# Performance work log

Hardware: AMD Instinct MI355X
Metric: run time of the kernel (lower is better)

The kernel has to match this reference:

```python
import jax, jax.numpy as jnp
import numpy as np

N = 50000      # nodes
E = 800000     # directed edges (avg degree 16)
F_IN = 128     # dataset.num_features
H = 256        # hidden_channels
C = 40         # dataset.num_classes


def _glorot(k, shape):
    lim = float(np.sqrt(6.0 / (shape[0] + shape[1])))
    return jax.random.uniform(k, shape, jnp.float32, -lim, lim)


def setup_inputs() -> dict:
    key = jax.random.key(0)
    ks = jax.random.split(key, 8)
    x = jax.random.normal(ks[0], (N, F_IN), jnp.float32)
    edge_index = jax.random.randint(ks[1], (2, E), 0, N, dtype=jnp.int32)
    W1 = _glorot(ks[2], (F_IN, H));      b1 = jnp.zeros((H,), jnp.float32)
    W2 = _glorot(ks[3], (H, H // 2));    b2 = jnp.zeros((H // 2,), jnp.float32)
    W3 = _glorot(ks[4], (H // 2, H // 4)); b3 = jnp.zeros((H // 4,), jnp.float32)
    W4 = _glorot(ks[5], (H // 4, C));    b4 = jnp.zeros((C,), jnp.float32)
    return {"x": x, "edge_index": edge_index,
            "W1": W1, "b1": b1, "W2": W2, "b2": b2,
            "W3": W3, "b3": b3, "W4": W4, "b4": b4}


def reference(x, edge_index, W1, b1, W2, b2, W3, b3, W4, b4):
    # GCNConv with default add_self_loops=True and symmetric normalization.
    loops = jnp.arange(N, dtype=edge_index.dtype)
    src = jnp.concatenate([edge_index[0], loops])   # message sources
    dst = jnp.concatenate([edge_index[1], loops])   # aggregation targets
    # degree computed on target index (PyG default), incl. self-loops
    deg = jax.ops.segment_sum(jnp.ones_like(dst, jnp.float32), dst, num_segments=N)
    dinv = jnp.where(deg > 0, jax.lax.rsqrt(deg), 0.0)
    norm = dinv[src] * dinv[dst]                    # [E+N]

    def conv(h, W, b):
        h = h @ W                                   # transform first (PyG order)
        msg = h[src] * norm[:, None]                # gather + scale
        return jax.ops.segment_sum(msg, dst, num_segments=N) + b

    h = jax.nn.relu(conv(x, W1, b1))   # dropout = identity in eval mode
    h = jax.nn.relu(conv(h, W2, b2))
    h = jax.nn.relu(conv(h, W3, b3))
    return conv(h, W4, b4)
```

## Files before the change

### kernel.cpp

```cpp
#include <hip/hip_runtime.h>
#include <stdint.h>

#define NNODES 50000
#define NEDGES 800000
#define NB ((NNODES + 255) / 256)
#define EPB 4096
#define SCAT_NBLK ((NEDGES + EPB - 1) / EPB)

typedef __attribute__((ext_vector_type(8))) short bf16x8;
typedef __attribute__((ext_vector_type(4))) float f32x4;

__device__ inline unsigned short f2bf(float f) {
    unsigned u = __float_as_uint(f);
    return (unsigned short)((u + 0x7fffu + ((u >> 16) & 1u)) >> 16);
}
__device__ inline float bf2f(unsigned short h) {
    return __uint_as_float(((unsigned)h) << 16);
}


__global__ void zero_kernel(int* __restrict__ p, int n) {
    int i = blockIdx.x * blockDim.x + threadIdx.x;
    if (i < n) p[i] = 0;
}

__global__ __launch_bounds__(256) void bucket_count_kernel(const int* __restrict__ dst,
                                                           int* __restrict__ bhist) {
    __shared__ int h[NB];
    for (int b = threadIdx.x; b < NB; b += 256) h[b] = 0;
    __syncthreads();
    const int base = blockIdx.x * EPB;
#pragma unroll
    for (int i = 0; i < EPB / 256; ++i) {
        const int e = base + threadIdx.x + i * 256;
        if (e < NEDGES) atomicAdd(&h[dst[e] >> 8], 1);
    }
    __syncthreads();
    for (int b = threadIdx.x; b < NB; b += 256)
        if (h[b]) atomicAdd(&bhist[b], h[b]);
}

__global__ __launch_bounds__(256) void bucket_scan_kernel(const int* __restrict__ bhist,
                                                          int* __restrict__ bofs,
                                                          int* __restrict__ gcur,
                                                          int* __restrict__ rp_last) {
    __shared__ int s[256];
    const int t = threadIdx.x;
    s[t] = (t < NB) ? bhist[t] : 0;
    __syncthreads();
    for (int off = 1; off < 256; off <<= 1) {
        int v = (t >= off) ? s[t - off] : 0;
        __syncthreads();
        s[t] += v;
        __syncthreads();
    }
    if (t < NB) {
        const int excl = (t > 0) ? s[t - 1] : 0;
        bofs[t] = excl;
        gcur[t] = excl;
    }
    if (t == 255) { bofs[NB] = s[255]; rp_last[0] = s[255]; }
}

__global__ __launch_bounds__(256) void bucket_scatter_kernel(const int* __restrict__ src,
                                                             const int* __restrict__ dst,
                                                             int* __restrict__ gcur,
                                                             unsigned* __restrict__ gpk) {
    __shared__ int h[256];
    __shared__ int s[256];
    __shared__ int gof[256];
    __shared__ unsigned pr[EPB];
    __shared__ int ga[EPB];

    const int t = threadIdx.x;
    const int base = blockIdx.x * EPB;
    const int nval = min(EPB, NEDGES - base);

    h[t] = 0;
    __syncthreads();
#pragma unroll
    for (int i = 0; i < EPB / 256; ++i) {
        const int e = base + t + i * 256;
        if (e < NEDGES) atomicAdd(&h[dst[e] >> 8], 1);
    }
    __syncthreads();
    s[t] = h[t];
    __syncthreads();
    for (int off = 1; off < 256; off <<= 1) {
        int v = (t >= off) ? s[t - off] : 0;
        __syncthreads();
        s[t] += v;
        __syncthreads();
    }
    {
        const int c = h[t];
        if (t < NB && c > 0) gof[t] = atomicAdd(&gcur[t], c);
        const int lofs = s[t] - c;
        h[t] = lofs;
        s[t] = lofs;
    }
    __syncthreads();
#pragma unroll
    for (int i = 0; i < EPB / 256; ++i) {
        const int e = base + t + i * 256;
        if (e < NEDGES) {
            const int d = dst[e];
            const int b = d >> 8;
            const int slot = atomicAdd(&h[b], 1);
            pr[slot] = ((unsigned)(d & 255) << 16) | (unsigned)src[e];
            ga[slot] = gof[b] + (slot - s[b]);
        }
    }
    __syncthreads();
#pragma unroll
    for (int i = 0; i < EPB / 256; ++i) {
        const int slot = t + i * 256;
        if (slot < nval) gpk[ga[slot]] = pr[slot];
    }
}

__global__ __launch_bounds__(256) void csr_fill_kernel(const unsigned* __restrict__ gpk,
                                                       const int* __restrict__ bofs,
                                                       int* __restrict__ rp,
                                                       float* __restrict__ dinv,
                                                       unsigned short* __restrict__ col,
                                                       const float* __restrict__ x,
                                                       unsigned short* __restrict__ xbf) {
    __shared__ int c[256];
    __shared__ int s[256];
    __shared__ int cur[256];
    __shared__ float sdv[256];
    const int t = threadIdx.x;
    const int b = blockIdx.x;
    const int beg = bofs[b], end = bofs[b + 1];
    c[t] = 0;
    __syncthreads();
    for (int e = beg + t; e < end; e += 256) atomicAdd(&c[gpk[e] >> 16], 1);
    __syncthreads();
    s[t] = c[t];
    __syncthreads();
    for (int off = 1; off < 256; off <<= 1) {
        int v = (t >= off) ? s[t - off] : 0;
        __syncthreads();
        s[t] += v;
        __syncthreads();
    }
    const int excl = s[t] - c[t];
    cur[t] = excl;
    const int node = b * 256 + t;
    const float dv = rsqrtf((float)(c[t] + 1));
    sdv[t] = dv;
    if (node < NNODES) {
        rp[node] = beg + excl;
        dinv[node] = dv;
    }
    __syncthreads();
    for (int e = beg + t; e < end; e += 256) {
        const unsigned p = gpk[e];
        const int r = atomicAdd(&cur[p >> 16], 1);
        col[beg + r] = (unsigned short)(p & 0xffffu);
    }
    const int nrows = min(256, NNODES - b * 256);
    const float* xb = x + (size_t)b * 256 * 128;
    unsigned short* ob = xbf + (size_t)b * 256 * 128;
    const int n4 = nrows * 32;
    for (int i = t; i < n4; i += 256) {
        const float dv2 = sdv[i >> 5];
        float4 v = *(const float4*)(xb + (size_t)i * 4);
        ushort4 hh;
        hh.x = f2bf(dv2 * v.x); hh.y = f2bf(dv2 * v.y);
        hh.z = f2bf(dv2 * v.z); hh.w = f2bf(dv2 * v.w);
        *(ushort4*)(ob + (size_t)i * 4) = hh;
    }
}


template <bool RELU, bool HAS_BIAS, bool WRITE_SPLIT>
__global__ __launch_bounds__(256) void agg128_kernel(const float* __restrict__ in32,
                                                     const unsigned short* __restrict__ inbf,
                                                     float* __restrict__ out,
                                                     unsigned short* __restrict__ outhi,
                                                     unsigned short* __restrict__ outlo,
                                                     const int* __restrict__ rp,
                                                     const unsigned short* __restrict__ col,
                                                     const float* __restrict__ dinv,
                                                     const float* __restrict__ bias) {
    const int wave = threadIdx.x >> 6;
    const int lane = threadIdx.x & 63;
    const int d = blockIdx.x * 4 + wave;
    if (d >= NNODES) return;
    const int quarter = lane >> 4;
    const int fl = lane & 15;
    const float dv = dinv[d];

    float acc[8] = {0.f, 0.f, 0.f, 0.f, 0.f, 0.f, 0.f, 0.f};
    if (quarter == 0) {
        float4 s0 = *(const float4*)(in32 + (size_t)d * 128 + fl * 8);
        float4 s1 = *(const float4*)(in32 + (size_t)d * 128 + fl * 8 + 4);
        acc[0] = dv * s0.x; acc[1] = dv * s0.y; acc[2] = dv * s0.z; acc[3] = dv * s0.w;
        acc[4] = dv * s1.x; acc[5] = dv * s1.y; acc[6] = dv * s1.z; acc[7] = dv * s1.w;
    }

    int j = rp[d] + quarter;
    const int end = rp[d + 1];
    for (; j + 12 < end; j += 16) {
        const int c0 = col[j], c1 = col[j + 4], c2 = col[j + 8], c3 = col[j + 12];
        bf16x8 a0 = *(const bf16x8*)(inbf + (size_t)c0 * 128 + fl * 8);
        bf16x8 a1 = *(const bf16x8*)(inbf + (size_t)c1 * 128 + fl * 8);
        bf16x8 a2 = *(const bf16x8*)(inbf + (size_t)c2 * 128 + fl * 8);
        bf16x8 a3 = *(const bf16x8*)(inbf + (size_t)c3 * 128 + fl * 8);
#pragma unroll
        for (int k = 0; k < 8; ++k)
            acc[k] += (bf2f((unsigned short)a0[k]) + bf2f((unsigned short)a1[k])) +
                      (bf2f((unsigned short)a2[k]) + bf2f((unsigned short)a3[k]));
    }
    for (; j + 4 < end; j += 8) {
        const int c0 = col[j], c1 = col[j + 4];
        bf16x8 a0 = *(const bf16x8*)(inbf + (size_t)c0 * 128 + fl * 8);
        bf16x8 a1 = *(const bf16x8*)(inbf + (size_t)c1 * 128 + fl * 8);
#pragma unroll
        for (int k = 0; k < 8; ++k)
            acc[k] += bf2f((unsigned short)a0[k]) + bf2f((unsigned short)a1[k]);
    }
    if (j < end) {
        const int c0 = col[j];
        bf16x8 a0 = *(const bf16x8*)(inbf + (size_t)c0 * 128 + fl * 8);
#pragma unroll
        for (int k = 0; k < 8; ++k) acc[k] += bf2f((unsigned short)a0[k]);
    }

#pragma unroll
    for (int v = 0; v < 8; ++v) {
        acc[v] += __shfl_down(acc[v], 32);
        acc[v] += __shfl_down(acc[v], 16);
    }

    if (quarter == 0) {
        float r[8];
#pragma unroll
        for (int v = 0; v < 8; ++v) {
            float t = dv * acc[v];
            if constexpr (HAS_BIAS) t += bias[fl * 8 + v];
            if constexpr (RELU) t = fmaxf(t, 0.0f);
            r[v] = t;
        }
        if constexpr (WRITE_SPLIT) {
            ushort4 h0, h1v, l0, l1v;
            h0.x = f2bf(r[0]); l0.x = f2bf(r[0] - bf2f(h0.x));
            h0.y = f2bf(r[1]); l0.y = f2bf(r[1] - bf2f(h0.y));
            h0.z = f2bf(r[2]); l0.z = f2bf(r[2] - bf2f(h0.z));
            h0.w = f2bf(r[3]); l0.w = f2bf(r[3] - bf2f(h0.w));
            h1v.x = f2bf(r[4]); l1v.x = f2bf(r[4] - bf2f(h1v.x));
            h1v.y = f2bf(r[5]); l1v.y = f2bf(r[5] - bf2f(h1v.y));
            h1v.z = f2bf(r[6]); l1v.z = f2bf(r[6] - bf2f(h1v.z));
            h1v.w = f2bf(r[7]); l1v.w = f2bf(r[7] - bf2f(h1v.w));
            *(ushort4*)(outhi + (size_t)d * 128 + fl * 8)     = h0;
            *(ushort4*)(outhi + (size_t)d * 128 + fl * 8 + 4) = h1v;
            *(ushort4*)(outlo + (size_t)d * 128 + fl * 8)     = l0;
            *(ushort4*)(outlo + (size_t)d * 128 + fl * 8 + 4) = l1v;
        } else {
            *(float4*)(out + (size_t)d * 128 + fl * 8)     = make_float4(r[0], r[1], r[2], r[3]);
            *(float4*)(out + (size_t)d * 128 + fl * 8 + 4) = make_float4(r[4], r[5], r[6], r[7]);
        }
    }
}

template <bool RELU, bool HAS_BIAS, bool WRITE_BF>
__global__ __launch_bounds__(256) void agg64_kernel(const float* __restrict__ in32,
                                                    const unsigned short* __restrict__ inbf,
                                                    float* __restrict__ out,
                                                    unsigned short* __restrict__ outbf,
                                                    const int* __restrict__ rp,
                                                    const unsigned short* __restrict__ col,
                                                    const float* __restrict__ dinv,
                                                    const float* __restrict__ bias) {
    const int wave = threadIdx.x >> 6;
    const int lane = threadIdx.x & 63;
    const int d = blockIdx.x * 4 + wave;
    if (d >= NNODES) return;
    const int eighth = lane >> 3;
    const int fl = lane & 7;
    const float dv = dinv[d];

    float acc[8] = {0.f, 0.f, 0.f, 0.f, 0.f, 0.f, 0.f, 0.f};
    if (eighth == 0) {
        float4 s0 = *(const float4*)(in32 + (size_t)d * 64 + fl * 8);
        float4 s1 = *(const float4*)(in32 + (size_t)d * 64 + fl * 8 + 4);
        acc[0] = dv * s0.x; acc[1] = dv * s0.y; acc[2] = dv * s0.z; acc[3] = dv * s0.w;
        acc[4] = dv * s1.x; acc[5] = dv * s1.y; acc[6] = dv * s1.z; acc[7] = dv * s1.w;
    }

    int j = rp[d] + eighth;
    const int end = rp[d + 1];
    for (; j + 8 < end; j += 16) {
        const int c0 = col[j], c1 = col[j + 8];
        bf16x8 a0 = *(const bf16x8*)(inbf + (size_t)c0 * 64 + fl * 8);
        bf16x8 a1 = *(const bf16x8*)(inbf + (size_t)c1 * 64 + fl * 8);
#pragma unroll
        for (int k = 0; k < 8; ++k)
            acc[k] += bf2f((unsigned short)a0[k]) + bf2f((unsigned short)a1[k]);
    }
    if (j < end) {
        const int c0 = col[j];
        bf16x8 a0 = *(const bf16x8*)(inbf + (size_t)c0 * 64 + fl * 8);
#pragma unroll
        for (int k = 0; k < 8; ++k) acc[k] += bf2f((unsigned short)a0[k]);
    }

#pragma unroll
    for (int v = 0; v < 8; ++v) {
        acc[v] += __shfl_down(acc[v], 32);
        acc[v] += __shfl_down(acc[v], 16);
        acc[v] += __shfl_down(acc[v], 8);
    }

    if (eighth == 0) {
        float r[8];
#pragma unroll
        for (int v = 0; v < 8; ++v) {
            float t = dv * acc[v];
            if constexpr (HAS_BIAS) t += bias[fl * 8 + v];
            if constexpr (RELU) t = fmaxf(t, 0.0f);
            r[v] = t;
        }
        *(float4*)(out + (size_t)d * 64 + fl * 8)     = make_float4(r[0], r[1], r[2], r[3]);
        *(float4*)(out + (size_t)d * 64 + fl * 8 + 4) = make_float4(r[4], r[5], r[6], r[7]);
        if constexpr (WRITE_BF) {
            ushort4 h0, h1;
            h0.x = f2bf(dv * r[0]); h0.y = f2bf(dv * r[1]);
            h0.z = f2bf(dv * r[2]); h0.w = f2bf(dv * r[3]);
            h1.x = f2bf(dv * r[4]); h1.y = f2bf(dv * r[5]);
            h1.z = f2bf(dv * r[6]); h1.w = f2bf(dv * r[7]);
            *(ushort4*)(outbf + (size_t)d * 64 + fl * 8)     = h0;
            *(ushort4*)(outbf + (size_t)d * 64 + fl * 8 + 4) = h1;
        }
    }
}


template <int K, int M>
__global__ __launch_bounds__(256) void repack_kernel(const float* __restrict__ W,
                                                     unsigned short* __restrict__ hi,
                                                     unsigned short* __restrict__ lo) {
    int i = blockIdx.x * 256 + threadIdx.x;
    if (i >= K * M) return;
    const int k = i / M, n = i % M;
    constexpr int KS = K / 32;
    const int cb = n >> 7;
    const int ct = (n >> 4) & 7;
    const int ln = ((k >> 3) & 3) * 16 + (n & 15);
    const int j  = k & 7;
    const int ks = k >> 5;
    const size_t o = ((((size_t)cb * KS + ks) * 8 + ct) * 64 + ln) * 8 + j;
    const float f = W[i];
    const unsigned short h = f2bf(f);
    hi[o] = h;
    lo[o] = f2bf(f - bf2f(h));
}


template <int K, int M, int EPI>
__global__ __launch_bounds__(256) void mfma2_kernel(const unsigned short* __restrict__ Ahi_g,
                                                    const unsigned short* __restrict__ Alo_g,
                                                    const unsigned short* __restrict__ Whi,
                                                    const unsigned short* __restrict__ Wlo,
                                                    const float* __restrict__ bias,
                                                    float* __restrict__ C,
                                                    unsigned short* __restrict__ Chi,
                                                    unsigned short* __restrict__ Clo,
                                                    unsigned short* __restrict__ Cbf,
                                                    const float* __restrict__ dinv) {
    constexpr int KS = K / 32;
    constexpr int CI = M / 64;
    __shared__ char lds[8192];
    char* Ahi = lds;
    char* Alo = lds + 4096;

    const int t = threadIdx.x;
    const int lane = t & 63;
    const int w = t >> 6;
    const int r0 = blockIdx.x * 64;
    const int quad = lane >> 4;
    const int cl = lane & 15;

    const size_t abase = ((size_t)(r0 + w * 16 + cl) * K + (size_t)quad * 8) * 2;

    f32x4 acc[4][CI];
#pragma unroll
    for (int i = 0; i < 4; ++i)
#pragma unroll
        for (int j = 0; j < CI; ++j) acc[i][j] = (f32x4){0.f, 0.f, 0.f, 0.f};

    for (int ks = 0; ks < KS; ++ks) {
        const size_t koff = abase + (size_t)ks * 64;
        __builtin_amdgcn_global_load_lds(
            (const __attribute__((address_space(1))) void*)((const char*)Ahi_g + koff),
            (__attribute__((address_space(3))) void*)(Ahi + w * 1024), 16, 0, 0);
        __builtin_amdgcn_global_load_lds(
            (const __attribute__((address_space(1))) void*)((const char*)Alo_g + koff),
            (__attribute__((address_space(3))) void*)(Alo + w * 1024), 16, 0, 0);

        bf16x8 bh[CI], bl[CI];
#pragma unroll
        for (int j = 0; j < CI; ++j) {
            const int g = w * CI + j;
            const size_t off = (size_t)(((g >> 3) * KS + ks) * 8 + (g & 7)) * 512 + lane * 8;
            bh[j] = *(const bf16x8*)(Whi + off);
            bl[j] = *(const bf16x8*)(Wlo + off);
        }
        __syncthreads();

        bf16x8 ah[4], al[4];
#pragma unroll
        for (int i = 0; i < 4; ++i) {
            ah[i] = *(const bf16x8*)(Ahi + i * 1024 + lane * 16);
            al[i] = *(const bf16x8*)(Alo + i * 1024 + lane * 16);
        }
#pragma unroll
        for (int i = 0; i < 4; ++i)
#pragma unroll
            for (int j = 0; j < CI; ++j) {
                acc[i][j] = __builtin_amdgcn_mfma_f32_16x16x32_bf16(ah[i], bh[j], acc[i][j], 0, 0, 0);
                acc[i][j] = __builtin_amdgcn_mfma_f32_16x16x32_bf16(ah[i], bl[j], acc[i][j], 0, 0, 0);
                acc[i][j] = __builtin_amdgcn_mfma_f32_16x16x32_bf16(al[i], bh[j], acc[i][j], 0, 0, 0);
            }
        __syncthreads();
    }

#pragma unroll
    for (int i = 0; i < 4; ++i)
#pragma unroll
        for (int j = 0; j < CI; ++j) {
            const int colg = (w * CI + j) * 16 + cl;
            float bv = 0.f;
            if constexpr (EPI == 0) bv = bias[colg];
#pragma unroll
            for (int r = 0; r < 4; ++r) {
                const int rowg = r0 + i * 16 + quad * 4 + r;
                if (rowg < NNODES) {
                    if constexpr (EPI == 0) {
                        const float v = fmaxf(acc[i][j][r] + bv, 0.f);
                        const unsigned short h = f2bf(v);
                        Chi[(size_t)rowg * M + colg] = h;
                        Clo[(size_t)rowg * M + colg] = f2bf(v - bf2f(h));
                    } else {
                        const float v = acc[i][j][r];
                        C[(size_t)rowg * M + colg] = v;
                        Cbf[(size_t)rowg * M + colg] = f2bf(dinv[rowg] * v);
                    }
                }
            }
        }
}


template <int BM, int BN, int BK, int TM, int TN, bool HAS_BIAS, bool RELU, bool WRITE_BF>
__global__ __launch_bounds__(256) void gemm_kernel(const float* __restrict__ A,
                                                   const float* __restrict__ W,
                                                   const float* __restrict__ bias,
                                                   float* __restrict__ C,
                                                   unsigned short* __restrict__ Cbf,
                                                   const float* __restrict__ dinv,
                                                   int Nrows, int K, int M) {
    constexpr int TX = BN / TN;
    constexpr int TY = BM / TM;
    static_assert(TX * TY == 256, "thread grid must be 256");
    constexpr int A_LOADS = (BM * BK) / (256 * 4);
    constexpr int W_LOADS = (BN * BK) / (256 * 4);
    static_assert(A_LOADS >= 1 && W_LOADS >= 1, "tile too small");

    const int tid = threadIdx.x;
    const int tx = tid % TX;
    const int ty = tid / TX;
    const int r0 = blockIdx.x * BM;
    const int c0 = blockIdx.y * BN;

    __shared__ float As[BK][BM + 4];
    __shared__ float Ws[BK][BN];

    float acc[TM][TN] = {};

    for (int k0 = 0; k0 < K; k0 += BK) {
#pragma unroll
        for (int l = 0; l < A_LOADS; ++l) {
            const int idx = tid + l * 256;
            const int row = idx / (BK / 4);
            const int kq = idx % (BK / 4);
            float4 v = make_float4(0.f, 0.f, 0.f, 0.f);
            const int gr = r0 + row;
            if (gr < Nrows) v = *(const float4*)(A + (size_t)gr * K + k0 + kq * 4);
            As[kq * 4 + 0][row] = v.x;
            As[kq * 4 + 1][row] = v.y;
            As[kq * 4 + 2][row] = v.z;
            As[kq * 4 + 3][row] = v.w;
        }
#pragma unroll
        for (int l = 0; l < W_LOADS; ++l) {
            const int idx = tid + l * 256;
            const int kk = idx / (BN / 4);
            const int cq = idx % (BN / 4);
            const int gc = c0 + cq * 4;
            float4 v;
            const float* wrow = W + (size_t)(k0 + kk) * M;
            if (gc + 3 < M) {
                v = *(const float4*)(wrow + gc);
            } else {
                v.x = (gc + 0 < M) ? wrow[gc + 0] : 0.f;
                v.y = (gc + 1 < M) ? wrow[gc + 1] : 0.f;
                v.z = (gc + 2 < M) ? wrow[gc + 2] : 0.f;
                v.w = (gc + 3 < M) ? wrow[gc + 3] : 0.f;
            }
            *(float4*)&Ws[kk][cq * 4] = v;
        }
        __syncthreads();

#pragma unroll
        for (int kk = 0; kk < BK; ++kk) {
            float a[TM], b[TN];
#pragma unroll
            for (int i = 0; i < TM; ++i) a[i] = As[kk][ty * TM + i];
#pragma unroll
            for (int j = 0; j < TN; ++j) b[j] = Ws[kk][tx * TN + j];
#pragma unroll
            for (int i = 0; i < TM; ++i)
#pragma unroll
                for (int j = 0; j < TN; ++j) acc[i][j] += a[i] * b[j];
        }
        __syncthreads();
    }

#pragma unroll
    for (int i = 0; i < TM; ++i) {
        const int gr = r0 + ty * TM + i;
        if (gr >= Nrows) continue;
        const float dvr = WRITE_BF ? dinv[gr] : 0.f;
#pragma unroll
        for (int j = 0; j < TN; ++j) {
            const int gc = c0 + tx * TN + j;
            if (gc >= M) continue;
            float v = acc[i][j];
            if constexpr (HAS_BIAS) v += bias[gc];
            if constexpr (RELU) v = fmaxf(v, 0.0f);
            C[(size_t)gr * M + gc] = v;
            if constexpr (WRITE_BF) Cbf[(size_t)gr * M + gc] = f2bf(dvr * v);
        }
    }
}


extern "C" void kernel_launch(void* const* d_in, const int* in_sizes, int n_in,
                              void* d_out, int out_size, void* d_ws, size_t ws_size,
                              hipStream_t stream) {
    const float* x  = (const float*)d_in[0];
    const int* ei   = (const int*)d_in[1];
    const float* W1 = (const float*)d_in[2];
    const float* b1 = (const float*)d_in[3];
    const float* W2 = (const float*)d_in[4];
    const float* b2 = (const float*)d_in[5];
    const float* W3 = (const float*)d_in[6];
    const float* b3 = (const float*)d_in[7];
    const float* W4 = (const float*)d_in[8];
    const float* b4 = (const float*)d_in[9];
    float* out = (float*)d_out;
    const int* esrc = ei;
    const int* edst = ei + NEDGES;

    char* w = (char*)d_ws;
    auto alloc = [&](size_t bytes) -> void* {
        void* p = (void*)w;
        w += (bytes + 255) & ~(size_t)255;
        return p;
    };
    int* rp     = (int*)alloc((size_t)(NNODES + 1) * 4);
    unsigned short* col = (unsigned short*)alloc((size_t)NEDGES * 2);
    float* dinv = (float*)alloc((size_t)NNODES * 4);
    int* bhist  = (int*)alloc((size_t)NB * 4);
    int* bofs   = (int*)alloc((size_t)(NB + 1) * 4);
    int* gcur   = (int*)alloc((size_t)NB * 4);
    unsigned* gpk = (unsigned*)alloc((size_t)NEDGES * 4);
    unsigned short* W1hi = (unsigned short*)alloc((size_t)128 * 256 * 2);
    unsigned short* W1lo = (unsigned short*)alloc((size_t)128 * 256 * 2);
    unsigned short* W2hi = (unsigned short*)alloc((size_t)256 * 128 * 2);
    unsigned short* W2lo = (unsigned short*)alloc((size_t)256 * 128 * 2);
    unsigned short* AggHi = (unsigned short*)alloc((size_t)NNODES * 128 * 2);
    unsigned short* AggLo = (unsigned short*)alloc((size_t)NNODES * 128 * 2);
    unsigned short* H1hi  = (unsigned short*)alloc((size_t)NNODES * 256 * 2);
    unsigned short* H1lo  = (unsigned short*)alloc((size_t)NNODES * 256 * 2);
    float* B0   = (float*)alloc((size_t)NNODES * 64 * 4);
    float* B1   = (float*)alloc((size_t)NNODES * 128 * 4);
    float* B2   = (float*)alloc((size_t)NNODES * 128 * 4);
    unsigned short* xbf  = (unsigned short*)alloc((size_t)NNODES * 128 * 2);
    unsigned short* B1bf = (unsigned short*)alloc((size_t)NNODES * 128 * 2);
    unsigned short* B0bf = (unsigned short*)alloc((size_t)NNODES * 64 * 2);
    unsigned short* B3bf = (unsigned short*)alloc((size_t)NNODES * 64 * 2);

    repack_kernel<128, 256><<<(128 * 256 + 255) / 256, 256, 0, stream>>>(W1, W1hi, W1lo);
    repack_kernel<256, 128><<<(256 * 128 + 255) / 256, 256, 0, stream>>>(W2, W2hi, W2lo);

    zero_kernel<<<1, 256, 0, stream>>>(bhist, NB);
    bucket_count_kernel<<<SCAT_NBLK, 256, 0, stream>>>(edst, bhist);
    bucket_scan_kernel<<<1, 256, 0, stream>>>(bhist, bofs, gcur, rp + NNODES);
    bucket_scatter_kernel<<<SCAT_NBLK, 256, 0, stream>>>(esrc, edst, gcur, gpk);
    csr_fill_kernel<<<NB, 256, 0, stream>>>(gpk, bofs, rp, dinv, col, x, xbf);

    const int aggGrid = (NNODES + 3) / 4;
    const int rowBlks64 = (NNODES + 63) / 64;

    agg128_kernel<false, false, true><<<aggGrid, 256, 0, stream>>>(
        x, xbf, nullptr, AggHi, AggLo, rp, col, dinv, nullptr);
    mfma2_kernel<128, 256, 0><<<rowBlks64, 256, 0, stream>>>(
        AggHi, AggLo, W1hi, W1lo, b1, nullptr, H1hi, H1lo, nullptr, nullptr);
    mfma2_kernel<256, 128, 1><<<rowBlks64, 256, 0, stream>>>(
        H1hi, H1lo, W2hi, W2lo, nullptr, B1, nullptr, nullptr, B1bf, dinv);
    agg128_kernel<true, true, false><<<aggGrid, 256, 0, stream>>>(
        B1, B1bf, B2, nullptr, nullptr, rp, col, dinv, b2);

    gemm_kernel<64, 64, 16, 4, 4, false, false, true>
        <<<dim3(rowBlks64, 1), 256, 0, stream>>>(B2, W3, nullptr, B0, B0bf, dinv, NNODES, 128, 64);
    agg64_kernel<true, true, true><<<aggGrid, 256, 0, stream>>>(B0, B0bf, B1, B3bf, rp, col, dinv, b3);

    agg64_kernel<false, false, false><<<aggGrid, 256, 0, stream>>>(B1, B3bf, B2, nullptr, rp, col, dinv, nullptr);
    gemm_kernel<64, 64, 16, 4, 4, true, false, false>
        <<<dim3(rowBlks64, 1), 256, 0, stream>>>(B2, W4, b4, out, nullptr, nullptr, NNODES, 64, 40);
}
```

Baseline: 355.5 us.

## Stage weight tiles in LDS and split MFMA GEMM over column blocks

The split-bf16 MFMA GEMM now loads weight fragments into LDS with global_load_lds instead of per-wave register loads from global memory. It also tiles the output columns in blocks of 128 via a 2D grid, so layer 1 launches twice as many blocks with half the accumulators each. The A tile is now loaded with coalesced ushort4 reads and row-bounds checks, then swizzled into LDS. The aim is more parallelism and lower register pressure for the larger GEMM, at the cost of extra LDS use and reading A twice in layer 1.

```diff
diff --git a/kernel.cpp b/kernel.cpp
--- a/kernel.cpp
+++ b/kernel.cpp
@@ -360,30 +360,32 @@
 
 
 template <int K, int M, int EPI>
-__global__ __launch_bounds__(256) void mfma2_kernel(const unsigned short* __restrict__ Ahi_g,
-                                                    const unsigned short* __restrict__ Alo_g,
-                                                    const unsigned short* __restrict__ Whi,
-                                                    const unsigned short* __restrict__ Wlo,
-                                                    const float* __restrict__ bias,
-                                                    float* __restrict__ C,
-                                                    unsigned short* __restrict__ Chi,
-                                                    unsigned short* __restrict__ Clo,
-                                                    unsigned short* __restrict__ Cbf,
-                                                    const float* __restrict__ dinv) {
+__global__ __launch_bounds__(256) void mfma_sb_kernel(const unsigned short* __restrict__ Ahi_g,
+                                                      const unsigned short* __restrict__ Alo_g,
+                                                      const unsigned short* __restrict__ Whi,
+                                                      const unsigned short* __restrict__ Wlo,
+                                                      const float* __restrict__ bias,
+                                                      float* __restrict__ C,
+                                                      unsigned short* __restrict__ Chi,
+                                                      unsigned short* __restrict__ Clo,
+                                                      unsigned short* __restrict__ Cbf,
+                                                      const float* __restrict__ dinv) {
     constexpr int KS = K / 32;
-    constexpr int CI = M / 64;
-    __shared__ char lds[8192];
+    constexpr int CI = 2;
+    __shared__ char lds[8192 + 16384];
     char* Ahi = lds;
     char* Alo = lds + 4096;
+    char* Bhi = lds + 8192;
+    char* Blo = lds + 16384;
 
     const int t = threadIdx.x;
     const int lane = t & 63;
     const int w = t >> 6;
     const int r0 = blockIdx.x * 64;
-    const int quad = lane >> 4;
-    const int cl = lane & 15;
-
-    const size_t abase = ((size_t)(r0 + w * 16 + cl) * K + (size_t)quad * 8) * 2;
+    const int n0 = blockIdx.y * 128;
+
+    const unsigned short* bhg = Whi + (size_t)blockIdx.y * KS * 4096;
+    const unsigned short* blg = Wlo + (size_t)blockIdx.y * KS * 4096;
 
     f32x4 acc[4][CI];
 #pragma unroll
@@ -392,29 +394,60 @@
         for (int j = 0; j < CI; ++j) acc[i][j] = (f32x4){0.f, 0.f, 0.f, 0.f};
 
     for (int ks = 0; ks < KS; ++ks) {
-        const size_t koff = abase + (size_t)ks * 64;
-        __builtin_amdgcn_global_load_lds(
-            (const __attribute__((address_space(1))) void*)((const char*)Ahi_g + koff),
-            (__attribute__((address_space(3))) void*)(Ahi + w * 1024), 16, 0, 0);
-        __builtin_amdgcn_global_load_lds(
-            (const __attribute__((address_space(1))) void*)((const char*)Alo_g + koff),
-            (__attribute__((address_space(3))) void*)(Alo + w * 1024), 16, 0, 0);
-
-        bf16x8 bh[CI], bl[CI];
-#pragma unroll
-        for (int j = 0; j < CI; ++j) {
-            const int g = w * CI + j;
-            const size_t off = (size_t)(((g >> 3) * KS + ks) * 8 + (g & 7)) * 512 + lane * 8;
-            bh[j] = *(const bf16x8*)(Whi + off);
-            bl[j] = *(const bf16x8*)(Wlo + off);
-        }
-        __syncthreads();
-
-        bf16x8 ah[4], al[4];
+        const int k0 = ks * 32;
+
+        {
+            const char* gh = (const char*)(bhg + (size_t)ks * 4096);
+            const char* gl = (const char*)(blg + (size_t)ks * 4096);
+#pragma unroll
+            for (int c = 0; c < 2; ++c) {
+                const int ct = w * 2 + c;
+                __builtin_amdgcn_global_load_lds(
+                    (const __attribute__((address_space(1))) void*)(gh + ct * 1024 + lane * 16),
+                    (__attribute__((address_space(3))) void*)(Bhi + ct * 1024), 16, 0, 0);
+                __builtin_amdgcn_global_load_lds(
+                    (const __attribute__((address_space(1))) void*)(gl + ct * 1024 + lane * 16),
+                    (__attribute__((address_space(3))) void*)(Blo + ct * 1024), 16, 0, 0);
+            }
+        }
+
+        ushort4 hv[2], lv[2];
+#pragma unroll
+        for (int i = 0; i < 2; ++i) {
+            const int q = t + i * 256;
+            const int row = q >> 3;
+            const int kq = (q & 7) * 4;
+            const int gr = r0 + row;
+            ushort4 h = {0, 0, 0, 0}, l = {0, 0, 0, 0};
+            if (gr < NNODES) {
+                h = *(const ushort4*)(Ahi_g + (size_t)gr * K + k0 + kq);
+                l = *(const ushort4*)(Alo_g + (size_t)gr * K + k0 + kq);
+            }
+            hv[i] = h;
+            lv[i] = l;
+        }
+#pragma unroll
+        for (int i = 0; i < 2; ++i) {
+            const int q = t + i * 256;
+            const int row = q >> 3;
+            const int kq = (q & 7) * 4;
+            const int rt = row >> 4, m = row & 15, quad = kq >> 3, j0 = kq & 7;
+            const int off = rt * 1024 + (quad * 16 + m) * 16 + j0 * 2;
+            *(ushort4*)(Ahi + off) = hv[i];
+            *(ushort4*)(Alo + off) = lv[i];
+        }
+        __syncthreads();
+
+        bf16x8 ah[4], al[4], bh[CI], bl[CI];
 #pragma unroll
         for (int i = 0; i < 4; ++i) {
             ah[i] = *(const bf16x8*)(Ahi + i * 1024 + lane * 16);
             al[i] = *(const bf16x8*)(Alo + i * 1024 + lane * 16);
+        }
+#pragma unroll
+        for (int j = 0; j < CI; ++j) {
+            bh[j] = *(const bf16x8*)(Bhi + (w * CI + j) * 1024 + lane * 16);
+            bl[j] = *(const bf16x8*)(Blo + (w * CI + j) * 1024 + lane * 16);
         }
 #pragma unroll
         for (int i = 0; i < 4; ++i)
@@ -427,11 +460,13 @@
         __syncthreads();
     }
 
-#pragma unroll
-    for (int i = 0; i < 4; ++i)
+    const int quad = lane >> 4;
+    const int cl = lane & 15;
+#pragma unroll
+    for (int i = 0; i < 4; ++i) {
 #pragma unroll
         for (int j = 0; j < CI; ++j) {
-            const int colg = (w * CI + j) * 16 + cl;
+            const int colg = n0 + w * (CI * 16) + j * 16 + cl;
             float bv = 0.f;
             if constexpr (EPI == 0) bv = bias[colg];
 #pragma unroll
@@ -451,6 +486,7 @@
                 }
             }
         }
+    }
 }
 
 
@@ -608,9 +644,9 @@
 
     agg128_kernel<false, false, true><<<aggGrid, 256, 0, stream>>>(
         x, xbf, nullptr, AggHi, AggLo, rp, col, dinv, nullptr);
-    mfma2_kernel<128, 256, 0><<<rowBlks64, 256, 0, stream>>>(
+    mfma_sb_kernel<128, 256, 0><<<dim3(rowBlks64, 2), 256, 0, stream>>>(
         AggHi, AggLo, W1hi, W1lo, b1, nullptr, H1hi, H1lo, nullptr, nullptr);
-    mfma2_kernel<256, 128, 1><<<rowBlks64, 256, 0, stream>>>(
+    mfma_sb_kernel<256, 128, 1><<<dim3(rowBlks64, 1), 256, 0, stream>>>(
         H1hi, H1lo, W2hi, W2lo, nullptr, B1, nullptr, nullptr, B1bf, dinv);
     agg128_kernel<true, true, false><<<aggGrid, 256, 0, stream>>>(
         B1, B1bf, B2, nullptr, nullptr, rp, col, dinv, b2);
```

After: 358.4 us. About the same (+0.8%).
